# Performance work log

Measured on AMD Instinct MI355X. Metric: run time of the kernel, lower is better.

Reference implementation:

```python
import jax, jax.numpy as jnp
import numpy as np
from jax import lax

B, T, H, V, P, L = 256, 100, 1024, 47, 3, 3
BEGIN_IDX = 1  # SmilesCharDictionary.begin_idx


def setup_inputs() -> dict:
    key = jax.random.key(0)
    ks = jax.random.split(key, 10)
    s = 0.05
    return {
        "x": jax.random.randint(ks[0], (B, T), 0, V),
        "properties": jax.random.normal(ks[1], (B, P), dtype=jnp.float32),
        "h0": jnp.zeros((L, B, H), jnp.float32),
        "c0": jnp.zeros((L, B, H), jnp.float32),
        "E": jax.random.normal(ks[2], (V, H), dtype=jnp.float32) * s,
        "W_ih0": jax.random.normal(ks[3], (4 * H, H + P), dtype=jnp.float32) * s,
        "W_hh0": jax.random.normal(ks[4], (4 * H, H), dtype=jnp.float32) * s,
        "b_ih0": jnp.zeros((4 * H,), jnp.float32),
        "b_hh0": jnp.zeros((4 * H,), jnp.float32),
        "W_ih_r": jax.random.normal(ks[5], (L - 1, 4 * H, H), dtype=jnp.float32) * s,
        "W_hh_r": jax.random.normal(ks[6], (L - 1, 4 * H, H), dtype=jnp.float32) * s,
        "b_ih_r": jnp.zeros((L - 1, 4 * H), jnp.float32),
        "b_hh_r": jnp.zeros((L - 1, 4 * H), jnp.float32),
        "W_dec": jax.random.normal(ks[7], (V, H), dtype=jnp.float32) * s,
        "b_dec": jnp.zeros((V,), jnp.float32),
        "seq_len": T,
    }


def _lstm_cell(gates, c):
    # PyTorch gate order: i, f, g, o
    i, f, g, o = jnp.split(gates, 4, axis=-1)
    i = jax.nn.sigmoid(i)
    f = jax.nn.sigmoid(f)
    o = jax.nn.sigmoid(o)
    g = jnp.tanh(g)
    c_new = f * c + i * g
    return o * jnp.tanh(c_new), c_new


def _forward(x, properties, h0, c0, E, W_ih0, W_hh0, b_ih0, b_hh0,
             W_ih_r, W_hh_r, b_ih_r, b_hh_r, W_dec, b_dec, seq_len):
    b = properties.shape[0]
    steps = seq_len - 1  # loop runs t = 1 .. seq_len-1
    # Teacher-forcing inputs: [begin, x[:,1], ..., x[:,seq_len-2]] (x[:,0] is unused)
    begin = jnp.full((b, 1), BEGIN_IDX, dtype=x.dtype)
    tokens = jnp.concatenate([begin, x[:, 1:seq_len - 1]], axis=1)  # [B, steps]
    emb = E[tokens]  # [B, steps, H]
    props = jnp.broadcast_to(properties[:, None, :], (b, steps, properties.shape[1]))
    inp0 = jnp.concatenate([emb, props], axis=-1)  # [B, steps, H+P]
    # Precompute layer-0 input contribution to the gates (one big GEMM)
    gx0 = jnp.einsum('bti,gi->btg', inp0, W_ih0) + b_ih0  # [B, steps, 4H]

    n_layers = h0.shape[0]

    def step(carry, gx_t):
        h, c = carry  # each [L, B, H]
        gates = gx_t + h[0] @ W_hh0.T + b_hh0
        h_new, c_new = _lstm_cell(gates, c[0])
        hs, cs = [h_new], [c_new]
        xl = h_new
        for l in range(n_layers - 1):
            gates = xl @ W_ih_r[l].T + b_ih_r[l] + h[l + 1] @ W_hh_r[l].T + b_hh_r[l]
            h_new, c_new = _lstm_cell(gates, c[l + 1])
            hs.append(h_new)
            cs.append(c_new)
            xl = h_new
        return (jnp.stack(hs), jnp.stack(cs)), xl

    (hT, cT), outs = lax.scan(step, (h0, c0), gx0.transpose(1, 0, 2))
    outs = outs.transpose(1, 0, 2)  # [B, steps, H]
    logits = jnp.einsum('bth,vh->btv', outs, W_dec) + b_dec  # [B, steps, V]
    return logits, hT, cT


def reference(x, properties, h0, c0, E, W_ih0, W_hh0, b_ih0, b_hh0,
              W_ih_r, W_hh_r, b_ih_r, b_hh_r, W_dec, b_dec, seq_len):
    return _forward(x, properties, h0, c0, E, W_ih0, W_hh0, b_ih0, b_hh0,
                    W_ih_r, W_hh_r, b_ih_r, b_hh_r, W_dec, b_dec, seq_len)
```

## Files before the change

### kernel.cpp

```cpp
#include <hip/hip_runtime.h>


typedef unsigned short u16;
typedef __bf16 bf16x8 __attribute__((ext_vector_type(8)));
typedef float f32x4 __attribute__((ext_vector_type(4)));
typedef u16 u16x8 __attribute__((ext_vector_type(8)));

#define MFMA16(a,b,c) __builtin_amdgcn_mfma_f32_16x16x32_bf16((a),(b),(c),0,0,0)
#define BH 262144

__device__ __forceinline__ u16 f2bf(float f){
  unsigned u = __builtin_bit_cast(unsigned, f);
  u += 0x7fffu + ((u >> 16) & 1u);
  return (u16)(u >> 16);
}
__device__ __forceinline__ float bf2f(u16 s){
  unsigned u = ((unsigned)s) << 16;
  return __builtin_bit_cast(float, u);
}
__device__ __forceinline__ float sigm(float x){ return 1.f/(1.f+__expf(-x)); }
__device__ __forceinline__ float tanhfast(float x){ return 1.f - 2.f/(__expf(2.f*x)+1.f); }

__device__ __forceinline__ void ld_lds16(const u16* g, u16* l){
  __builtin_amdgcn_global_load_lds((const __attribute__((address_space(1))) void*)g,
                                   (__attribute__((address_space(3))) void*)l, 16, 0, 0);
}

__global__ void k_conv(const float* __restrict__ src, u16* __restrict__ dst,
                       long total, int srow, int sstride, int dstride, int doff){
  long i = ((long)blockIdx.x*blockDim.x + threadIdx.x)*8;
  if (i >= total) return;
  long r = i / srow;
  int  k = (int)(i - r*srow);
  const float* s = src + r*(long)sstride + k;
  u16x8 o;
  #pragma unroll
  for (int j=0;j<8;++j) o[j] = f2bf(s[j]);
  *(u16x8*)(dst + r*(long)dstride + doff + k) = o;
}

__global__ void k_repackB(const float* __restrict__ Wih, const float* __restrict__ Whh,
                          u16* __restrict__ dst, int nkt){
  long p = (long)blockIdx.x*256 + threadIdx.x;
  int G = (int)(p & 511);
  long q = p >> 9;
  int kt = (int)(q % nkt);
  int jt = (int)(q / nkt);
  int r = G >> 3, s = G & 7;
  int kk = kt*64 + ((s ^ (r & 7)) << 3);
  int n = (r >> 4)*1024 + jt*16 + (r & 15);
  const float* src = (kk < 1024) ? Wih + (size_t)n*1024 + kk
                                 : Whh + (size_t)n*1024 + (kk - 1024);
  u16x8 o;
  #pragma unroll
  for (int j=0;j<8;++j) o[j] = f2bf(src[j]);
  *(u16x8*)(dst + p*8) = o;
}

__global__ void k_misc(const float* __restrict__ b_ih0, const float* __restrict__ b_hh0,
                       const float* __restrict__ b_ihr, const float* __restrict__ b_hhr,
                       const float* __restrict__ h0, const float* __restrict__ c0,
                       const float* __restrict__ props, const float* __restrict__ W_ih0,
                       u16* __restrict__ Ebf, u16* __restrict__ Wdec,
                       float* __restrict__ bias0, float* __restrict__ bcat,
                       u16* __restrict__ hist0, u16* __restrict__ hist1,
                       u16* __restrict__ outsbF,
                       float* __restrict__ cst, float* __restrict__ gxp){
  long i = (long)blockIdx.x*256 + threadIdx.x;
  if (i < 4096){ bias0[i] = b_ih0[i] + b_hh0[i]; return; }
  i -= 4096;
  if (i < 2*4096){ bcat[i] = b_ihr[i] + b_hhr[i]; return; }
  i -= 2*4096;
  if (i < 1024){ Ebf[47*1024 + i] = 0; Wdec[47*1024 + i] = 0; return; }
  i -= 1024;
  if (i < (long)3*BH){
    int l = (int)(i >> 18); long r = i & (BH-1);
    u16 v = f2bf(h0[i]);
    if (l==0)      hist0[(size_t)7*BH + r] = v;
    else if (l==1) hist1[(size_t)7*BH + r] = v;
    else           outsbF[r] = v;
    cst[i] = c0[i];
    return;
  }
  i -= (long)3*BH;
  if (i < (long)256*4096){
    int b = (int)(i >> 12), n = (int)(i & 4095);
    const float* wr = W_ih0 + (long)n*1027 + 1024;
    gxp[i] = props[b*3+0]*wr[0] + props[b*3+1]*wr[1] + props[b*3+2]*wr[2];
  }
}

__global__ __launch_bounds__(64)
void k_gxemb(const u16* __restrict__ Ebf, const u16* __restrict__ Wih0b, float* __restrict__ gxe){
  const int lane = threadIdx.x;
  const int cl = lane & 15, ko = (lane >> 4)*8;
  const int m0 = blockIdx.x*16;
  const int n0 = blockIdx.y*16;
  f32x4 acc = {0.f,0.f,0.f,0.f};
  const u16* ap = Ebf   + (size_t)(m0+cl)*1024 + ko;
  const u16* bp = Wih0b + (size_t)(n0+cl)*1024 + ko;
  for (int k0=0; k0<1024; k0+=32){
    bf16x8 a = *(const bf16x8*)(ap + k0);
    bf16x8 b = *(const bf16x8*)(bp + k0);
    acc = MFMA16(a, b, acc);
  }
  const int rbase = (lane >> 4)*4;
  #pragma unroll
  for (int q=0;q<4;++q){
    int v = m0 + rbase + q;
    if (v < 47) gxe[(size_t)v*4096 + n0 + cl] = acc[q];
  }
}

#define KLOOP_BODY(APTR_EXPR)                                                   \
  auto stage = [&](int s, int kt){                                              \
    const int kbase = kt*64;                                                    \
    u16* sA = lds + (size_t)s*12288;                                            \
    u16* sB = sA + 8192;                                                        \
    _Pragma("unroll")                                                           \
    for (int j=0;j<4;++j){                                                      \
      int G = j*256 + tid; int r = G >> 3;                                      \
      int kk = kbase + (((G & 7) ^ (r & 7)) << 3);                              \
      ld_lds16(APTR_EXPR, sA + (size_t)G*8);                                    \
    }                                                                           \
    _Pragma("unroll")                                                           \
    for (int j=0;j<2;++j){                                                      \
      int G = j*256 + tid;                                                      \
      ld_lds16(Bblk + (size_t)kt*4096 + (size_t)G*8, sB + (size_t)G*8);         \
    }                                                                           \
  };                                                                            \
  f32x4 acc[2][4];                                                              \
  _Pragma("unroll")                                                             \
  for (int mf=0; mf<2; ++mf)                                                    \
    _Pragma("unroll")                                                           \
    for (int g=0; g<4; ++g) acc[mf][g] = (f32x4){0.f,0.f,0.f,0.f};              \
  stage(0,0); stage(1,1);                                                       \
  for (int kt=0; kt<16; ++kt){                                                  \
    if (kt == 15) asm volatile("s_waitcnt vmcnt(0)" ::: "memory");              \
    else          asm volatile("s_waitcnt vmcnt(6)" ::: "memory");              \
    __builtin_amdgcn_s_barrier();                                               \
    asm volatile("" ::: "memory");                                              \
    if (kt+2 < 16) stage((kt+2)%3, kt+2);                                       \
    const u16* A = lds + (size_t)(kt%3)*12288;                                  \
    const u16* B = A + 8192;                                                    \
    __builtin_amdgcn_s_setprio(1);                                              \
    _Pragma("unroll")                                                           \
    for (int half=0; half<2; ++half){                                           \
      const int kg = half*4 + hi;                                               \
      bf16x8 a0, a1, b[4];                                                      \
      { int r = m0w + cl;      a0 = *(const bf16x8*)(A + r*64 + ((kg ^ (r&7))<<3)); } \
      { int r = m0w + 16 + cl; a1 = *(const bf16x8*)(A + r*64 + ((kg ^ (r&7))<<3)); } \
      _Pragma("unroll")                                                         \
      for (int g=0; g<4; ++g){                                                  \
        int r = g*16 + cl;                                                      \
        b[g] = *(const bf16x8*)(B + r*64 + ((kg ^ (r&7))<<3));                  \
      }                                                                         \
      _Pragma("unroll")                                                         \
      for (int g=0; g<4; ++g){                                                  \
        acc[0][g] = MFMA16(a0, b[g], acc[0][g]);                                \
        acc[1][g] = MFMA16(a1, b[g], acc[1][g]);                                \
      }                                                                         \
    }                                                                           \
    __builtin_amdgcn_s_setprio(0);                                              \
    asm volatile("" ::: "memory");                                              \
  }

template<int LAYER>
__device__ __forceinline__ void diagh_tile(int mt, int jt, int t,
    const int* __restrict__ x, const u16* hp, u16* aux, float* cc,
    const u16* __restrict__ Bblk, const float* __restrict__ bias,
    const float* __restrict__ gxe, const float* __restrict__ gxp,
    const u16* xpt, u16* lds)
{
  const int tid = threadIdx.x;
  const int lane = tid & 63, w = tid >> 6;
  const int cl = lane & 15, hi = lane >> 4;
  const int m_base = mt*128, m0w = w*32;

  KLOOP_BODY(hp + (size_t)(m_base + r)*1024 + kk)

  const int hcol = jt*16 + cl;
  const float bi_ = bias[hcol], bf_ = bias[1024+hcol],
              bg_ = bias[2048+hcol], bo_ = bias[3072+hcol];
  #pragma unroll
  for (int mf=0; mf<2; ++mf){
    #pragma unroll
    for (int q=0; q<4; ++q){
      const int row = m_base + m0w + mf*16 + hi*4 + q;
      float gi = acc[mf][0][q] + bi_;
      float gf = acc[mf][1][q] + bf_;
      float gg = acc[mf][2][q] + bg_;
      float go = acc[mf][3][q] + bo_;
      if (LAYER == 0){
        const int tok = (t==0) ? 1 : x[row*100 + t];
        const float* ge = gxe + (size_t)tok*4096;
        const float* gp = gxp + (size_t)row*4096;
        gi += ge[hcol]        + gp[hcol];
        gf += ge[1024 + hcol] + gp[1024 + hcol];
        gg += ge[2048 + hcol] + gp[2048 + hcol];
        go += ge[3072 + hcol] + gp[3072 + hcol];
      } else {
        const u16* xr = xpt + (size_t)row*4096;
        gi += bf2f(xr[hcol]);
        gf += bf2f(xr[1024 + hcol]);
        gg += bf2f(xr[2048 + hcol]);
        go += bf2f(xr[3072 + hcol]);
      }
      const float i_ = sigm(gi), f_ = sigm(gf), o_ = sigm(go), g_ = tanhfast(gg);
      const size_t off = (size_t)row*1024 + hcol;
      const float cn = f_*cc[off] + i_*g_;
      cc[off] = cn;
      aux[off] = f2bf(o_*tanhfast(cn));
    }
  }
}

__global__ __launch_bounds__(256)
void k_diag(int d, const int* __restrict__ x, u16* hist0, u16* hist1, u16* outsbF,
            float* __restrict__ cst, const u16* __restrict__ WpkH,
            const float* __restrict__ bias0, const float* __restrict__ bcat,
            const float* __restrict__ gxe, const float* __restrict__ gxp,
            const u16* __restrict__ xp1, const u16* __restrict__ xp2)
{
  extern __shared__ u16 lds[];
  const int id = blockIdx.x;
  const int mt = id / 192;
  const int slot = id - mt*192;
  const int layer = slot >> 6;
  const int jt = slot & 63;
  const int t = d - 4*layer;
  if (t < 0 || t > 98) return;
  if (layer == 0){
    diagh_tile<0>(mt, jt, t, x, hist0 + (size_t)((t+7)&7)*BH, hist0 + (size_t)(t&7)*BH,
                  cst, WpkH + (size_t)jt*65536, bias0, gxe, gxp, nullptr, lds);
  } else if (layer == 1){
    const u16* xpt = xp1 + (size_t)((((t>>2)&1)<<2) + (t&3))*1048576;
    diagh_tile<1>(mt, jt, t, x, hist1 + (size_t)((t+7)&7)*BH, hist1 + (size_t)(t&7)*BH,
                  cst + BH, WpkH + (size_t)4194304 + (size_t)jt*65536, bcat,
                  nullptr, nullptr, xpt, lds);
  } else {
    const u16* xpt = xp2 + (size_t)((((t>>2)&1)<<2) + (t&3))*1048576;
    diagh_tile<2>(mt, jt, t, x, outsbF + (size_t)t*BH, outsbF + (size_t)(t+1)*BH,
                  cst + 2*BH, WpkH + (size_t)8388608 + (size_t)jt*65536, bcat + 4096,
                  nullptr, nullptr, xpt, lds);
  }
}

__global__ __launch_bounds__(256)
void k_xp(int w, const u16* __restrict__ hist, const u16* __restrict__ Wblk,
          u16* __restrict__ xpout)
{
  extern __shared__ u16 lds[];
  const int id = blockIdx.x;
  const int mt = id >> 6, jt = id & 63;
  const int tid = threadIdx.x;
  const int lane = tid & 63, wv = tid >> 6;
  const int cl = lane & 15, hi = lane >> 4;
  const int tprime = mt >> 1;
  const int m_base = (mt & 1)*128, m0w = wv*32;
  const u16* hp = hist + (size_t)((4*w + tprime) & 7)*BH;
  const u16* Bblk = Wblk + (size_t)jt*65536;

  KLOOP_BODY(hp + (size_t)(m_base + r)*1024 + kk)

  const int hcol = jt*16 + cl;
  u16* xpo = xpout + (size_t)(((w&1)<<2) + tprime)*1048576;
  #pragma unroll
  for (int mf=0; mf<2; ++mf){
    #pragma unroll
    for (int q=0; q<4; ++q){
      const int m = m_base + m0w + mf*16 + hi*4 + q;
      u16* xr = xpo + (size_t)m*4096 + hcol;
      xr[0]    = f2bf(acc[mf][0][q]);
      xr[1024] = f2bf(acc[mf][1][q]);
      xr[2048] = f2bf(acc[mf][2][q]);
      xr[3072] = f2bf(acc[mf][3][q]);
    }
  }
}

__global__ __launch_bounds__(256)
void k_decode(const u16* __restrict__ outs, const u16* __restrict__ Wdec,
              const float* __restrict__ bdec, float* __restrict__ logits){
  const int lane = threadIdx.x & 63, w = threadIdx.x >> 6;
  const int cl = lane & 15, ko = (lane >> 4)*8;
  const size_t m0 = ((size_t)blockIdx.x*4 + w)*16;
  const u16* ap = outs + (m0+cl)*1024 + ko;
  f32x4 acc[3];
  #pragma unroll
  for (int nt=0; nt<3; ++nt) acc[nt] = (f32x4){0.f,0.f,0.f,0.f};
  const u16* bp = Wdec + (size_t)cl*1024 + ko;
  for (int k0=0; k0<1024; k0+=32){
    bf16x8 a = *(const bf16x8*)(ap + k0);
    #pragma unroll
    for (int nt=0; nt<3; ++nt){
      bf16x8 b = *(const bf16x8*)(bp + (size_t)nt*16*1024 + k0);
      acc[nt] = MFMA16(a, b, acc[nt]);
    }
  }
  const int rbase = (lane >> 4)*4;
  #pragma unroll
  for (int nt=0; nt<3; ++nt){
    #pragma unroll
    for (int q=0; q<4; ++q){
      int v = nt*16 + cl;
      if (v < 47){
        size_t row = m0 + rbase + q;
        int tt = (int)(row >> 8);
        int b  = (int)(row & 255);
        logits[((size_t)b*99 + tt)*47 + v] = acc[nt][q] + bdec[v];
      }
    }
  }
}

__global__ void k_final(const u16* __restrict__ h0s, const u16* __restrict__ h1s,
                        const u16* __restrict__ h2s, const float* __restrict__ cst,
                        float* __restrict__ out){
  long i = (long)blockIdx.x*256 + threadIdx.x;
  if (i < (long)3*BH){
    int l = (int)(i >> 18); long r = i & (BH-1);
    const u16* src = (l==0) ? h0s : (l==1) ? h1s : h2s;
    out[1191168 + i] = bf2f(src[r]);
    out[1191168 + 786432 + i] = cst[i];
  }
}

extern "C" void kernel_launch(void* const* d_in, const int* in_sizes, int n_in,
                              void* d_out, int out_size, void* d_ws, size_t ws_size,
                              hipStream_t stream) {
  (void)in_sizes; (void)n_in; (void)out_size; (void)ws_size;
  const int*   x      = (const int*)  d_in[0];
  const float* props  = (const float*)d_in[1];
  const float* h0     = (const float*)d_in[2];
  const float* c0     = (const float*)d_in[3];
  const float* E      = (const float*)d_in[4];
  const float* W_ih0  = (const float*)d_in[5];
  const float* W_hh0  = (const float*)d_in[6];
  const float* b_ih0  = (const float*)d_in[7];
  const float* b_hh0  = (const float*)d_in[8];
  const float* W_ih_r = (const float*)d_in[9];
  const float* W_hh_r = (const float*)d_in[10];
  const float* b_ih_r = (const float*)d_in[11];
  const float* b_hh_r = (const float*)d_in[12];
  const float* W_dec  = (const float*)d_in[13];
  const float* b_dec  = (const float*)d_in[14];
  float* out = (float*)d_out;

  u16* WpkH   = (u16*)d_ws;
  u16* WpkI   = WpkH  + (size_t)12582912;
  u16* Wdec   = WpkI  + (size_t)8388608;
  u16* Ebf    = Wdec  + (size_t)49152;
  u16* hist0  = Ebf   + (size_t)49152;
  u16* hist1  = hist0 + (size_t)8*BH;
  u16* outsbF = hist1 + (size_t)8*BH;
  u16* xp1    = outsbF + (size_t)100*BH;
  u16* xp2    = xp1   + (size_t)8388608;
  u16* Wih0b  = xp1;
  float* gxe   = (float*)(xp2 + (size_t)8388608);
  float* gxp   = gxe   + (size_t)196608;
  float* bias0 = gxp   + (size_t)1048576;
  float* bcat  = bias0 + 4096;
  float* cst   = bcat  + 8192;

  k_repackB<<<2048, 256, 0, stream>>>(W_hh0, W_hh0, WpkH, 16);
  k_repackB<<<2048, 256, 0, stream>>>(W_hh_r, W_hh_r, WpkH + (size_t)4194304, 16);
  k_repackB<<<2048, 256, 0, stream>>>(W_hh_r + (size_t)4194304, W_hh_r + (size_t)4194304,
                                      WpkH + (size_t)8388608, 16);
  k_repackB<<<2048, 256, 0, stream>>>(W_ih_r, W_ih_r, WpkI, 16);
  k_repackB<<<2048, 256, 0, stream>>>(W_ih_r + (size_t)4194304, W_ih_r + (size_t)4194304,
                                      WpkI + (size_t)4194304, 16);
  k_conv<<<2048, 256, 0, stream>>>(W_ih0, Wih0b, (long)4096*1024, 1024, 1027, 1024, 0);
  k_conv<<<24,   256, 0, stream>>>(E,     Ebf,   (long)47*1024,   1024, 1024, 1024, 0);
  k_conv<<<24,   256, 0, stream>>>(W_dec, Wdec,  (long)47*1024,   1024, 1024, 1024, 0);
  k_misc<<<7221, 256, 0, stream>>>(b_ih0, b_hh0, b_ih_r, b_hh_r, h0, c0, props, W_ih0,
                                   Ebf, Wdec, bias0, bcat, hist0, hist1, outsbF, cst, gxp);
  k_gxemb<<<dim3(3,256), 64, 0, stream>>>(Ebf, Wih0b, gxe);

  (void)hipFuncSetAttribute(reinterpret_cast<const void*>(k_diag),
                            hipFuncAttributeMaxDynamicSharedMemorySize, 73728);
  (void)hipFuncSetAttribute(reinterpret_cast<const void*>(k_xp),
                            hipFuncAttributeMaxDynamicSharedMemorySize, 73728);
  for (int d = 0; d < 107; ++d){
    k_diag<<<384, 256, 73728, stream>>>(d, x, hist0, hist1, outsbF, cst,
                                        WpkH, bias0, bcat, gxe, gxp, xp1, xp2);
    if (d >= 3 && ((d-3) & 3) == 0){
      int w = (d-3) >> 2;
      if (w < 25) k_xp<<<512, 256, 73728, stream>>>(w, hist0, WpkI, xp1);
    }
    if (d >= 7 && ((d-7) & 3) == 0){
      int w = (d-7) >> 2;
      if (w < 25) k_xp<<<512, 256, 73728, stream>>>(w, hist1, WpkI + (size_t)4194304, xp2);
    }
  }

  k_decode<<<396, 256, 0, stream>>>(outsbF + (size_t)BH, Wdec, b_dec, out);
  k_final<<<3072, 256, 0, stream>>>(hist0 + (size_t)2*BH, hist1 + (size_t)2*BH,
                                    outsbF + (size_t)99*BH, cst, out);
}
```

Before: 2.758 ms.

## Fold input-projection GEMM tiles into the diagonal wavefront kernel with 2-step batching

Stops launching separate k_xp kernels every four diagonals and instead appends 256 extra blocks to each k_diag launch, which compute the layer-1/2 input projections for two timesteps. The layer offset in the wavefront shrinks from 4 to 3 diagonals, so there are fewer total diagonals and fewer kernel launches, and the projection work overlaps with the recurrent tiles. The xp buffers are halved. The risk is a heavier per-diagonal launch (640 blocks), which could lengthen the critical path when the grid exceeds one wave.

Measured after the change: 2.475 ms, median of 2. 1.11x faster.

```diff
diff --git a/kernel.cpp b/kernel.cpp
--- a/kernel.cpp
+++ b/kernel.cpp
@@ -215,56 +215,17 @@
   }
 }
 
-__global__ __launch_bounds__(256)
-void k_diag(int d, const int* __restrict__ x, u16* hist0, u16* hist1, u16* outsbF,
-            float* __restrict__ cst, const u16* __restrict__ WpkH,
-            const float* __restrict__ bias0, const float* __restrict__ bcat,
-            const float* __restrict__ gxe, const float* __restrict__ gxp,
-            const u16* __restrict__ xp1, const u16* __restrict__ xp2)
+__device__ __forceinline__ void xp_tile(int m_base, int jt,
+    const u16* hp, const u16* __restrict__ Bblk, u16* xpo, u16* lds)
 {
-  extern __shared__ u16 lds[];
-  const int id = blockIdx.x;
-  const int mt = id / 192;
-  const int slot = id - mt*192;
-  const int layer = slot >> 6;
-  const int jt = slot & 63;
-  const int t = d - 4*layer;
-  if (t < 0 || t > 98) return;
-  if (layer == 0){
-    diagh_tile<0>(mt, jt, t, x, hist0 + (size_t)((t+7)&7)*BH, hist0 + (size_t)(t&7)*BH,
-                  cst, WpkH + (size_t)jt*65536, bias0, gxe, gxp, nullptr, lds);
-  } else if (layer == 1){
-    const u16* xpt = xp1 + (size_t)((((t>>2)&1)<<2) + (t&3))*1048576;
-    diagh_tile<1>(mt, jt, t, x, hist1 + (size_t)((t+7)&7)*BH, hist1 + (size_t)(t&7)*BH,
-                  cst + BH, WpkH + (size_t)4194304 + (size_t)jt*65536, bcat,
-                  nullptr, nullptr, xpt, lds);
-  } else {
-    const u16* xpt = xp2 + (size_t)((((t>>2)&1)<<2) + (t&3))*1048576;
-    diagh_tile<2>(mt, jt, t, x, outsbF + (size_t)t*BH, outsbF + (size_t)(t+1)*BH,
-                  cst + 2*BH, WpkH + (size_t)8388608 + (size_t)jt*65536, bcat + 4096,
-                  nullptr, nullptr, xpt, lds);
-  }
-}
-
-__global__ __launch_bounds__(256)
-void k_xp(int w, const u16* __restrict__ hist, const u16* __restrict__ Wblk,
-          u16* __restrict__ xpout)
-{
-  extern __shared__ u16 lds[];
-  const int id = blockIdx.x;
-  const int mt = id >> 6, jt = id & 63;
   const int tid = threadIdx.x;
-  const int lane = tid & 63, wv = tid >> 6;
+  const int lane = tid & 63, w = tid >> 6;
   const int cl = lane & 15, hi = lane >> 4;
-  const int tprime = mt >> 1;
-  const int m_base = (mt & 1)*128, m0w = wv*32;
-  const u16* hp = hist + (size_t)((4*w + tprime) & 7)*BH;
-  const u16* Bblk = Wblk + (size_t)jt*65536;
+  const int m0w = w*32;
 
   KLOOP_BODY(hp + (size_t)(m_base + r)*1024 + kk)
 
   const int hcol = jt*16 + cl;
-  u16* xpo = xpout + (size_t)(((w&1)<<2) + tprime)*1048576;
   #pragma unroll
   for (int mf=0; mf<2; ++mf){
     #pragma unroll
@@ -276,6 +237,51 @@
       xr[2048] = f2bf(acc[mf][2][q]);
       xr[3072] = f2bf(acc[mf][3][q]);
     }
+  }
+}
+
+__global__ __launch_bounds__(256)
+void k_diag(int d, const int* __restrict__ x, u16* hist0, u16* hist1, u16* outsbF,
+            float* __restrict__ cst, const u16* __restrict__ WpkH,
+            const u16* __restrict__ WpkI,
+            const float* __restrict__ bias0, const float* __restrict__ bcat,
+            const float* __restrict__ gxe, const float* __restrict__ gxp,
+            u16* __restrict__ xpb1, u16* __restrict__ xpb2)
+{
+  extern __shared__ u16 lds[];
+  const int id = blockIdx.x;
+  if (id < 384){
+    const int mt = id / 192;
+    const int slot = id - mt*192;
+    const int layer = slot >> 6;
+    const int jt = slot & 63;
+    const int t = d - 3*layer;
+    if (t < 0 || t > 98) return;
+    if (layer == 0){
+      diagh_tile<0>(mt, jt, t, x, hist0 + (size_t)((t+7)&7)*BH, hist0 + (size_t)(t&7)*BH,
+                    cst, WpkH + (size_t)jt*65536, bias0, gxe, gxp, nullptr, lds);
+    } else if (layer == 1){
+      const u16* xpt = xpb1 + (size_t)((((t>>1)&1)<<1) + (t&1))*1048576;
+      diagh_tile<1>(mt, jt, t, x, hist1 + (size_t)((t+7)&7)*BH, hist1 + (size_t)(t&7)*BH,
+                    cst + BH, WpkH + (size_t)4194304 + (size_t)jt*65536, bcat,
+                    nullptr, nullptr, xpt, lds);
+    } else {
+      const u16* xpt = xpb2 + (size_t)((((t>>1)&1)<<1) + (t&1))*1048576;
+      diagh_tile<2>(mt, jt, t, x, outsbF + (size_t)t*BH, outsbF + (size_t)(t+1)*BH,
+                    cst + 2*BH, WpkH + (size_t)8388608 + (size_t)jt*65536, bcat + 4096,
+                    nullptr, nullptr, xpt, lds);
+    }
+  } else {
+    const int idx = id - 384;
+    const int mtx = idx >> 6, jt = idx & 63;
+    const int tsub = mtx >> 1, m_base = (mtx & 1)*128;
+    int w; const u16* hist; const u16* Wblk; u16* xpo;
+    if ((d & 1) == 0){ w = (d-2)>>1; hist = hist0; Wblk = WpkI;                     xpo = xpb1; }
+    else             { w = (d-5)>>1; hist = hist1; Wblk = WpkI + (size_t)4194304;   xpo = xpb2; }
+    const int t = 2*w + tsub;
+    if (t > 98) return;
+    xp_tile(m_base, jt, hist + (size_t)(t&7)*BH, Wblk + (size_t)jt*65536,
+            xpo + (size_t)(((w&1)<<1) + tsub)*1048576, lds);
   }
 }
 
@@ -354,10 +360,10 @@
   u16* hist0  = Ebf   + (size_t)49152;
   u16* hist1  = hist0 + (size_t)8*BH;
   u16* outsbF = hist1 + (size_t)8*BH;
-  u16* xp1    = outsbF + (size_t)100*BH;
-  u16* xp2    = xp1   + (size_t)8388608;
-  u16* Wih0b  = xp1;
-  float* gxe   = (float*)(xp2 + (size_t)8388608);
+  u16* xpb1   = outsbF + (size_t)100*BH;
+  u16* xpb2   = xpb1  + (size_t)4194304;
+  u16* Wih0b  = xpb1;
+  float* gxe   = (float*)(xpb2 + (size_t)4194304);
   float* gxp   = gxe   + (size_t)196608;
   float* bias0 = gxp   + (size_t)1048576;
   float* bcat  = bias0 + 4096;
@@ -379,19 +385,11 @@
 
   (void)hipFuncSetAttribute(reinterpret_cast<const void*>(k_diag),
                             hipFuncAttributeMaxDynamicSharedMemorySize, 73728);
-  (void)hipFuncSetAttribute(reinterpret_cast<const void*>(k_xp),
-                            hipFuncAttributeMaxDynamicSharedMemorySize, 73728);
-  for (int d = 0; d < 107; ++d){
-    k_diag<<<384, 256, 73728, stream>>>(d, x, hist0, hist1, outsbF, cst,
-                                        WpkH, bias0, bcat, gxe, gxp, xp1, xp2);
-    if (d >= 3 && ((d-3) & 3) == 0){
-      int w = (d-3) >> 2;
-      if (w < 25) k_xp<<<512, 256, 73728, stream>>>(w, hist0, WpkI, xp1);
-    }
-    if (d >= 7 && ((d-7) & 3) == 0){
-      int w = (d-7) >> 2;
-      if (w < 25) k_xp<<<512, 256, 73728, stream>>>(w, hist1, WpkI + (size_t)4194304, xp2);
-    }
+  for (int d = 0; d <= 104; ++d){
+    bool hx = ((d & 1) == 0) ? (d >= 2 && d <= 100) : (d >= 5 && d <= 103);
+    k_diag<<<384 + (hx ? 256 : 0), 256, 73728, stream>>>(
+        d, x, hist0, hist1, outsbF, cst, WpkH, WpkI,
+        bias0, bcat, gxe, gxp, xpb1, xpb2);
   }
 
   k_decode<<<396, 256, 0, stream>>>(outsbF + (size_t)BH, Wdec, b_dec, out);
```
